# Kernel tuning notes

Hardware: AMD Instinct MI355X
Metric: run time of the kernel (lower is better)

Reference implementation:

```python
import jax, jax.numpy as jnp
import numpy as np

N_NODES = 100000
N_EDGES = 1600000
IN_F = 256
OUT_F = 128


def setup_inputs() -> dict:
    key = jax.random.key(0)
    ks = jax.random.split(key, 6)
    stdv = 1.0 / np.sqrt(OUT_F)
    x = jax.random.normal(ks[0], (N_NODES, IN_F), dtype=jnp.float32)
    edge_row = jax.random.randint(ks[1], (N_EDGES,), 0, N_NODES)
    edge_col = jax.random.randint(ks[2], (N_EDGES,), 0, N_NODES)
    edge_val = jax.random.uniform(ks[3], (N_EDGES,), dtype=jnp.float32)
    weight = jax.random.uniform(ks[4], (IN_F, OUT_F), minval=-stdv, maxval=stdv, dtype=jnp.float32)
    bias = jax.random.uniform(ks[5], (OUT_F,), minval=-stdv, maxval=stdv, dtype=jnp.float32)
    return {"x": x, "edge_row": edge_row, "edge_col": edge_col,
            "edge_val": edge_val, "weight": weight, "bias": bias}


def reference(x, edge_row, edge_col, edge_val, weight, bias):
    # support = input @ W                       [N, out]
    support = x @ weight
    # output = spmm(adj, support): for each edge (r, c, v),
    # out[r] += v * support[c]  -- gather then segment-sum over destinations.
    gathered = support[edge_col] * edge_val[:, None]   # [E, out]
    out = jax.ops.segment_sum(gathered, edge_row, num_segments=N_NODES)
    return out + bias
```

## Files before the change

### kernel.cpp

```cpp
#include <hip/hip_runtime.h>
#include <hip/hip_bf16.h>

#define N_NODES 100000
#define N_EDGES 1600000
#define IN_F 256
#define OUT_F 128

#define NBUCK 782
#define CH 4096
#define NCHB ((N_EDGES + CH - 1) / CH)
#define HCAP 2048
#define BCAP 3072

typedef __attribute__((ext_vector_type(8))) short bhalf8;
typedef __attribute__((ext_vector_type(4))) float f32x4;

static __device__ __forceinline__ unsigned short f2bfs(float f) {
    __hip_bfloat16 h = __float2bfloat16(f);
    return *reinterpret_cast<unsigned short*>(&h);
}

__global__ __launch_bounds__(256) void wt_kernel(
    const float* __restrict__ W, unsigned short* __restrict__ Wt)
{
    const int idx = blockIdx.x * 256 + threadIdx.x;
    const int col = idx >> 8;
    const int k   = idx & 255;
    Wt[idx] = f2bfs(W[(size_t)k * OUT_F + col]);
}

__global__ __launch_bounds__(512) void gemm_mfma_kernel(
    const float* __restrict__ x, const unsigned short* __restrict__ Wt,
    unsigned short* __restrict__ support)
{
    __shared__ unsigned short Bs[128 * 256];

    const int tid = threadIdx.x;

    {
        const int row = tid >> 2;
        const int q   = tid & 3;
        const uint4* src = (const uint4*)(Wt + (size_t)row * 256);
        uint4* dst       = (uint4*)(Bs + (size_t)row * 256);
        const int sw = row & 7;
        #pragma unroll
        for (int i = q * 8; i < q * 8 + 8; ++i)
            dst[i ^ sw] = src[i];
    }
    __syncthreads();

    const int wave = tid >> 6, lane = tid & 63;
    const int r_lo = lane & 15;
    const int kq   = lane >> 4;
    const int row0 = blockIdx.x * 128 + wave * 16;
    const int row  = row0 + r_lo;

    const float* xa = x + (size_t)min(row, N_NODES - 1) * IN_F + kq * 8;

    f32x4 acc[8];
    #pragma unroll
    for (int c = 0; c < 8; ++c) acc[c] = (f32x4)0.f;

    #pragma unroll
    for (int ks = 0; ks < 8; ++ks) {
        const float4 al = *(const float4*)(xa + ks * 32);
        const float4 ah = *(const float4*)(xa + ks * 32 + 4);

        bhalf8 A;
        A[0] = (short)f2bfs(al.x); A[1] = (short)f2bfs(al.y);
        A[2] = (short)f2bfs(al.z); A[3] = (short)f2bfs(al.w);
        A[4] = (short)f2bfs(ah.x); A[5] = (short)f2bfs(ah.y);
        A[6] = (short)f2bfs(ah.z); A[7] = (short)f2bfs(ah.w);

        #pragma unroll
        for (int cf = 0; cf < 8; ++cf) {
            const int col = cf * 16 + r_lo;
            const int off = ((ks * 32 + kq * 8) ^ ((col & 7) << 3));
            const bhalf8 B = *(const bhalf8*)(Bs + (size_t)col * 256 + off);
            acc[cf] = __builtin_amdgcn_mfma_f32_16x16x32_bf16(B, A, acc[cf], 0, 0, 0);
        }
    }

    if (row < N_NODES) {
        unsigned short* dst = support + (size_t)row * OUT_F + kq * 4;
        #pragma unroll
        for (int cf = 0; cf < 8; ++cf) {
            ushort4 s4;
            s4.x = f2bfs(acc[cf][0]);
            s4.y = f2bfs(acc[cf][1]);
            s4.z = f2bfs(acc[cf][2]);
            s4.w = f2bfs(acc[cf][3]);
            *(ushort4*)(dst + cf * 16) = s4;
        }
    }
}

__global__ __launch_bounds__(512) void bscatter_kernel(
    const int* __restrict__ erow, const int* __restrict__ ecol,
    const float* __restrict__ eval, int* __restrict__ bcnt,
    int2* __restrict__ ebuf)
{
    __shared__ int h[NBUCK];
    __shared__ int cur[NBUCK];
    __shared__ int gbase[NBUCK];
    __shared__ int ps[512];
    __shared__ unsigned short bb[CH];
    __shared__ int2 buf[CH];

    const int tid = threadIdx.x;
    const int e0  = blockIdx.x * CH;
    const int e1  = min(e0 + CH, N_EDGES);
    const int n   = e1 - e0;

    for (int i = tid; i < NBUCK; i += 512) h[i] = 0;
    __syncthreads();

    for (int e = e0 + tid; e < e1; e += 512)
        atomicAdd(&h[erow[e] >> 7], 1);
    __syncthreads();

    {
        const int idx0 = tid * 2;
        int sum = 0;
        #pragma unroll
        for (int k = 0; k < 2; ++k) { const int ii = idx0 + k; if (ii < NBUCK) sum += h[ii]; }
        ps[tid] = sum;
        __syncthreads();
        for (int off = 1; off < 512; off <<= 1) {
            const int a  = (tid >= off) ? ps[tid - off] : 0;
            const int x0 = ps[tid];
            __syncthreads();
            ps[tid] = x0 + a;
            __syncthreads();
        }
        int run = (tid == 0) ? 0 : ps[tid - 1];
        #pragma unroll
        for (int k = 0; k < 2; ++k) {
            const int ii = idx0 + k;
            if (ii < NBUCK) { cur[ii] = run; run += h[ii]; }
        }
    }
    __syncthreads();

    for (int e = e0 + tid; e < e1; e += 512) {
        const int r = erow[e];
        const int b = r >> 7;
        const int p = atomicAdd(&cur[b], 1);
        buf[p] = make_int2(((r & 127) << 17) | ecol[e], __float_as_int(eval[e]));
        bb[p]  = (unsigned short)b;
    }
    __syncthreads();

    for (int i = tid; i < NBUCK; i += 512)
        gbase[i] = h[i] ? (i * BCAP + atomicAdd(&bcnt[i], h[i])) : 0;
    __syncthreads();

    for (int i = tid; i < n; i += 512) {
        const int b  = bb[i];
        const int lb = cur[b] - h[b];
        ebuf[gbase[b] + (i - lb)] = buf[i];
    }
}

__global__ __launch_bounds__(256) void hspmm_kernel(
    const int* __restrict__ bcnt, const int2* __restrict__ ebuf,
    const unsigned short* __restrict__ support,
    const float* __restrict__ bias, float* __restrict__ out)
{
    __shared__ int2 srt[HCAP];
    __shared__ int rc[64];
    __shared__ int rb[65];
    __shared__ int cc[64];

    const int blk = blockIdx.x;
    const int pb  = blk >> 1;
    const unsigned hf = blk & 1;
    const int row0 = (pb << 7) + ((int)hf << 6);
    if (row0 >= N_NODES) return;
    const int nrows = min(64, N_NODES - row0);

    const int tid  = threadIdx.x;
    const int lane = tid & 63;
    const int grp  = tid >> 4;
    const int l4   = tid & 15;

    const int beg = pb * BCAP;
    const int end = beg + bcnt[pb];

    if (tid < 64) rc[tid] = 0;
    __syncthreads();

    for (int i = beg + tid; i < end; i += 256) {
        const unsigned ex = (unsigned)ebuf[i].x;
        const unsigned lr7 = (ex >> 17) & 127u;
        if ((lr7 >> 6) == hf) atomicAdd(&rc[lr7 & 63], 1);
    }
    __syncthreads();

    if (tid < 64) {
        int v = rc[tid];
        #pragma unroll
        for (int off = 1; off < 64; off <<= 1) {
            const int t = __shfl_up(v, off);
            if (lane >= off) v += t;
        }
        rb[tid + 1] = v;
        cc[tid] = v - rc[tid];
        if (tid == 0) rb[0] = 0;
    }
    __syncthreads();

    for (int i = beg + tid; i < end; i += 256) {
        const int2 e = ebuf[i];
        const unsigned lr7 = ((unsigned)e.x >> 17) & 127u;
        if ((lr7 >> 6) == hf)
            srt[atomicAdd(&cc[lr7 & 63], 1)] = e;
    }
    __syncthreads();

#define ACC(V, U)                                            \
    a0 += (V) * __uint_as_float((U).x << 16);                \
    a1 += (V) * __uint_as_float((U).x & 0xFFFF0000u);        \
    a2 += (V) * __uint_as_float((U).y << 16);                \
    a3 += (V) * __uint_as_float((U).y & 0xFFFF0000u);        \
    a4 += (V) * __uint_as_float((U).z << 16);                \
    a5 += (V) * __uint_as_float((U).z & 0xFFFF0000u);        \
    a6 += (V) * __uint_as_float((U).w << 16);                \
    a7 += (V) * __uint_as_float((U).w & 0xFFFF0000u);

    const float4 bv0 = *(const float4*)(bias + l4 * 8);
    const float4 bv1 = *(const float4*)(bias + l4 * 8 + 4);

    for (int lr = grp; lr < nrows; lr += 16) {
        const int s  = rb[lr];
        const int t2 = rb[lr + 1];
        float a0 = 0.f, a1 = 0.f, a2 = 0.f, a3 = 0.f;
        float a4 = 0.f, a5 = 0.f, a6 = 0.f, a7 = 0.f;
        int j = s;
        for (; j + 4 <= t2; j += 4) {
            const int2 e0 = srt[j],     e1 = srt[j + 1];
            const int2 e2 = srt[j + 2], e3 = srt[j + 3];
            const uint4 u0 = *(const uint4*)(support + ((size_t)(e0.x & 0x1FFFF) << 7) + l4 * 8);
            const uint4 u1 = *(const uint4*)(support + ((size_t)(e1.x & 0x1FFFF) << 7) + l4 * 8);
            const uint4 u2 = *(const uint4*)(support + ((size_t)(e2.x & 0x1FFFF) << 7) + l4 * 8);
            const uint4 u3 = *(const uint4*)(support + ((size_t)(e3.x & 0x1FFFF) << 7) + l4 * 8);
            const float v0 = __int_as_float(e0.y), v1 = __int_as_float(e1.y);
            const float v2 = __int_as_float(e2.y), v3 = __int_as_float(e3.y);
            ACC(v0, u0) ACC(v1, u1) ACC(v2, u2) ACC(v3, u3)
        }
        for (; j < t2; ++j) {
            const int2 e = srt[j];
            const uint4 u = *(const uint4*)(support + ((size_t)(e.x & 0x1FFFF) << 7) + l4 * 8);
            const float v = __int_as_float(e.y);
            ACC(v, u)
        }
        float4* o = (float4*)(out + ((size_t)(row0 + lr) << 7) + l4 * 8);
        o[0] = make_float4(a0 + bv0.x, a1 + bv0.y, a2 + bv0.z, a3 + bv0.w);
        o[1] = make_float4(a4 + bv1.x, a5 + bv1.y, a6 + bv1.z, a7 + bv1.w);
    }
#undef ACC
}

extern "C" void kernel_launch(void* const* d_in, const int* in_sizes, int n_in,
                              void* d_out, int out_size, void* d_ws, size_t ws_size,
                              hipStream_t stream) {
    const float* x    = (const float*)d_in[0];
    const int*   erow = (const int*)  d_in[1];
    const int*   ecol = (const int*)  d_in[2];
    const float* eval = (const float*)d_in[3];
    const float* W    = (const float*)d_in[4];
    const float* bias = (const float*)d_in[5];
    float*       out  = (float*)d_out;

    char* ws = (char*)d_ws;
    unsigned short* support = (unsigned short*)ws; ws += (size_t)N_NODES * OUT_F * 2;
    unsigned short* Wt      = (unsigned short*)ws; ws += (size_t)OUT_F * IN_F * 2;
    int*  bcnt  = (int*)ws;                        ws += 3136;
    int2* ebuf  = (int2*)ws;                       ws += (size_t)NBUCK * BCAP * 8;

    hipMemsetAsync(bcnt, 0, NBUCK * 4, stream);

    wt_kernel<<<(OUT_F * IN_F) / 256, 256, 0, stream>>>(W, Wt);
    gemm_mfma_kernel<<<(N_NODES + 127) / 128, 512, 0, stream>>>(x, Wt, support);

    bscatter_kernel<<<NCHB, 512, 0, stream>>>(erow, ecol, eval, bcnt, ebuf);

    hspmm_kernel<<<NBUCK * 2, 256, 0, stream>>>(bcnt, ebuf, support, bias, out);
}
```

Before: 135.3 us.

## Merge GEMM and edge bucket-scatter into one heterogeneous launch

Combines the MFMA GEMM kernel and the edge bucket-scatter kernel into a single launch. The first block range does the scatter and the rest do the GEMM, sharing one 64KB shared-memory union. The two independent stages can then run concurrently on the GPU and one kernel-launch boundary goes away. In exchange, every block reserves the full 64KB of shared memory, which can lower occupancy for the scatter blocks.

```diff
diff --git a/kernel.cpp b/kernel.cpp
--- a/kernel.cpp
+++ b/kernel.cpp
@@ -8,7 +8,8 @@
 
 #define NBUCK 782
 #define CH 4096
-#define NCHB ((N_EDGES + CH - 1) / CH)
+#define NSCAT ((N_EDGES + CH - 1) / CH)
+#define NGEMM ((N_NODES + 127) / 128)
 #define HCAP 2048
 #define BCAP 3072
 
@@ -29,136 +30,135 @@
     Wt[idx] = f2bfs(W[(size_t)k * OUT_F + col]);
 }
 
-__global__ __launch_bounds__(512) void gemm_mfma_kernel(
+__global__ __launch_bounds__(512) void fused_kernel(
     const float* __restrict__ x, const unsigned short* __restrict__ Wt,
-    unsigned short* __restrict__ support)
-{
-    __shared__ unsigned short Bs[128 * 256];
-
-    const int tid = threadIdx.x;
-
-    {
-        const int row = tid >> 2;
-        const int q   = tid & 3;
-        const uint4* src = (const uint4*)(Wt + (size_t)row * 256);
-        uint4* dst       = (uint4*)(Bs + (size_t)row * 256);
-        const int sw = row & 7;
-        #pragma unroll
-        for (int i = q * 8; i < q * 8 + 8; ++i)
-            dst[i ^ sw] = src[i];
-    }
-    __syncthreads();
-
-    const int wave = tid >> 6, lane = tid & 63;
-    const int r_lo = lane & 15;
-    const int kq   = lane >> 4;
-    const int row0 = blockIdx.x * 128 + wave * 16;
-    const int row  = row0 + r_lo;
-
-    const float* xa = x + (size_t)min(row, N_NODES - 1) * IN_F + kq * 8;
-
-    f32x4 acc[8];
-    #pragma unroll
-    for (int c = 0; c < 8; ++c) acc[c] = (f32x4)0.f;
-
-    #pragma unroll
-    for (int ks = 0; ks < 8; ++ks) {
-        const float4 al = *(const float4*)(xa + ks * 32);
-        const float4 ah = *(const float4*)(xa + ks * 32 + 4);
-
-        bhalf8 A;
-        A[0] = (short)f2bfs(al.x); A[1] = (short)f2bfs(al.y);
-        A[2] = (short)f2bfs(al.z); A[3] = (short)f2bfs(al.w);
-        A[4] = (short)f2bfs(ah.x); A[5] = (short)f2bfs(ah.y);
-        A[6] = (short)f2bfs(ah.z); A[7] = (short)f2bfs(ah.w);
-
-        #pragma unroll
-        for (int cf = 0; cf < 8; ++cf) {
-            const int col = cf * 16 + r_lo;
-            const int off = ((ks * 32 + kq * 8) ^ ((col & 7) << 3));
-            const bhalf8 B = *(const bhalf8*)(Bs + (size_t)col * 256 + off);
-            acc[cf] = __builtin_amdgcn_mfma_f32_16x16x32_bf16(B, A, acc[cf], 0, 0, 0);
-        }
-    }
-
-    if (row < N_NODES) {
-        unsigned short* dst = support + (size_t)row * OUT_F + kq * 4;
-        #pragma unroll
-        for (int cf = 0; cf < 8; ++cf) {
-            ushort4 s4;
-            s4.x = f2bfs(acc[cf][0]);
-            s4.y = f2bfs(acc[cf][1]);
-            s4.z = f2bfs(acc[cf][2]);
-            s4.w = f2bfs(acc[cf][3]);
-            *(ushort4*)(dst + cf * 16) = s4;
-        }
-    }
-}
-
-__global__ __launch_bounds__(512) void bscatter_kernel(
+    unsigned short* __restrict__ support,
     const int* __restrict__ erow, const int* __restrict__ ecol,
     const float* __restrict__ eval, int* __restrict__ bcnt,
     int2* __restrict__ ebuf)
 {
-    __shared__ int h[NBUCK];
-    __shared__ int cur[NBUCK];
-    __shared__ int gbase[NBUCK];
-    __shared__ int ps[512];
-    __shared__ unsigned short bb[CH];
-    __shared__ int2 buf[CH];
-
+    __shared__ __align__(16) char smem[65536];
     const int tid = threadIdx.x;
-    const int e0  = blockIdx.x * CH;
-    const int e1  = min(e0 + CH, N_EDGES);
-    const int n   = e1 - e0;
-
-    for (int i = tid; i < NBUCK; i += 512) h[i] = 0;
-    __syncthreads();
-
-    for (int e = e0 + tid; e < e1; e += 512)
-        atomicAdd(&h[erow[e] >> 7], 1);
-    __syncthreads();
-
-    {
-        const int idx0 = tid * 2;
-        int sum = 0;
+
+    if (blockIdx.x < NSCAT) {
+        int2*           buf   = (int2*)smem;
+        unsigned short* bb    = (unsigned short*)(smem + 32768);
+        int*            h     = (int*)(smem + 40960);
+        int*            cur   = (int*)(smem + 44096);
+        int*            gbase = (int*)(smem + 47232);
+        int*            ps    = (int*)(smem + 50368);
+
+        const int e0 = blockIdx.x * CH;
+        const int e1 = min(e0 + CH, N_EDGES);
+        const int n  = e1 - e0;
+
+        for (int i = tid; i < NBUCK; i += 512) h[i] = 0;
+        __syncthreads();
+
+        for (int e = e0 + tid; e < e1; e += 512)
+            atomicAdd(&h[erow[e] >> 7], 1);
+        __syncthreads();
+
+        {
+            const int idx0 = tid * 2;
+            int sum = 0;
+            #pragma unroll
+            for (int k = 0; k < 2; ++k) { const int ii = idx0 + k; if (ii < NBUCK) sum += h[ii]; }
+            ps[tid] = sum;
+            __syncthreads();
+            for (int off = 1; off < 512; off <<= 1) {
+                const int a  = (tid >= off) ? ps[tid - off] : 0;
+                const int x0 = ps[tid];
+                __syncthreads();
+                ps[tid] = x0 + a;
+                __syncthreads();
+            }
+            int run = (tid == 0) ? 0 : ps[tid - 1];
+            #pragma unroll
+            for (int k = 0; k < 2; ++k) {
+                const int ii = idx0 + k;
+                if (ii < NBUCK) { cur[ii] = run; run += h[ii]; }
+            }
+        }
+        __syncthreads();
+
+        for (int e = e0 + tid; e < e1; e += 512) {
+            const int r = erow[e];
+            const int b = r >> 7;
+            const int p = atomicAdd(&cur[b], 1);
+            buf[p] = make_int2(((r & 127) << 17) | ecol[e], __float_as_int(eval[e]));
+            bb[p]  = (unsigned short)b;
+        }
+        __syncthreads();
+
+        for (int i = tid; i < NBUCK; i += 512)
+            gbase[i] = h[i] ? (i * BCAP + atomicAdd(&bcnt[i], h[i])) : 0;
+        __syncthreads();
+
+        for (int i = tid; i < n; i += 512) {
+            const int b  = bb[i];
+            const int lb = cur[b] - h[b];
+            ebuf[gbase[b] + (i - lb)] = buf[i];
+        }
+    } else {
+        unsigned short* Bs = (unsigned short*)smem;
+
+        {
+            const int row = tid >> 2;
+            const int q   = tid & 3;
+            const uint4* src = (const uint4*)(Wt + (size_t)row * 256);
+            uint4* dst       = (uint4*)(Bs + (size_t)row * 256);
+            const int sw = row & 7;
+            #pragma unroll
+            for (int i = q * 8; i < q * 8 + 8; ++i)
+                dst[i ^ sw] = src[i];
+        }
+        __syncthreads();
+
+        const int wave = tid >> 6, lane = tid & 63;
+        const int r_lo = lane & 15;
+        const int kq   = lane >> 4;
+        const int row0 = (blockIdx.x - NSCAT) * 128 + wave * 16;
+        const int row  = row0 + r_lo;
+
+        const float* xa = x + (size_t)min(row, N_NODES - 1) * IN_F + kq * 8;
+
+        f32x4 acc[8];
         #pragma unroll
-        for (int k = 0; k < 2; ++k) { const int ii = idx0 + k; if (ii < NBUCK) sum += h[ii]; }
-        ps[tid] = sum;
-        __syncthreads();
-        for (int off = 1; off < 512; off <<= 1) {
-            const int a  = (tid >= off) ? ps[tid - off] : 0;
-            const int x0 = ps[tid];
-            __syncthreads();
-            ps[tid] = x0 + a;
-            __syncthreads();
-        }
-        int run = (tid == 0) ? 0 : ps[tid - 1];
+        for (int c = 0; c < 8; ++c) acc[c] = (f32x4)0.f;
+
         #pragma unroll
-        for (int k = 0; k < 2; ++k) {
-            const int ii = idx0 + k;
-            if (ii < NBUCK) { cur[ii] = run; run += h[ii]; }
-        }
-    }
-    __syncthreads();
-
-    for (int e = e0 + tid; e < e1; e += 512) {
-        const int r = erow[e];
-        const int b = r >> 7;
-        const int p = atomicAdd(&cur[b], 1);
-        buf[p] = make_int2(((r & 127) << 17) | ecol[e], __float_as_int(eval[e]));
-        bb[p]  = (unsigned short)b;
-    }
-    __syncthreads();
-
-    for (int i = tid; i < NBUCK; i += 512)
-        gbase[i] = h[i] ? (i * BCAP + atomicAdd(&bcnt[i], h[i])) : 0;
-    __syncthreads();
-
-    for (int i = tid; i < n; i += 512) {
-        const int b  = bb[i];
-        const int lb = cur[b] - h[b];
-        ebuf[gbase[b] + (i - lb)] = buf[i];
+        for (int ks = 0; ks < 8; ++ks) {
+            const float4 al = *(const float4*)(xa + ks * 32);
+            const float4 ah = *(const float4*)(xa + ks * 32 + 4);
+
+            bhalf8 A;
+            A[0] = (short)f2bfs(al.x); A[1] = (short)f2bfs(al.y);
+            A[2] = (short)f2bfs(al.z); A[3] = (short)f2bfs(al.w);
+            A[4] = (short)f2bfs(ah.x); A[5] = (short)f2bfs(ah.y);
+            A[6] = (short)f2bfs(ah.z); A[7] = (short)f2bfs(ah.w);
+
+            #pragma unroll
+            for (int cf = 0; cf < 8; ++cf) {
+                const int col = cf * 16 + r_lo;
+                const int off = ((ks * 32 + kq * 8) ^ ((col & 7) << 3));
+                const bhalf8 B = *(const bhalf8*)(Bs + (size_t)col * 256 + off);
+                acc[cf] = __builtin_amdgcn_mfma_f32_16x16x32_bf16(B, A, acc[cf], 0, 0, 0);
+            }
+        }
+
+        if (row < N_NODES) {
+            unsigned short* dst = support + (size_t)row * OUT_F + kq * 4;
+            #pragma unroll
+            for (int cf = 0; cf < 8; ++cf) {
+                ushort4 s4;
+                s4.x = f2bfs(acc[cf][0]);
+                s4.y = f2bfs(acc[cf][1]);
+                s4.z = f2bfs(acc[cf][2]);
+                s4.w = f2bfs(acc[cf][3]);
+                *(ushort4*)(dst + cf * 16) = s4;
+            }
+        }
     }
 }
 
@@ -281,9 +281,9 @@
     hipMemsetAsync(bcnt, 0, NBUCK * 4, stream);
 
     wt_kernel<<<(OUT_F * IN_F) / 256, 256, 0, stream>>>(W, Wt);
-    gemm_mfma_kernel<<<(N_NODES + 127) / 128, 512, 0, stream>>>(x, Wt, support);
-
-    bscatter_kernel<<<NCHB, 512, 0, stream>>>(erow, ecol, eval, bcnt, ebuf);
+
+    fused_kernel<<<NSCAT + NGEMM, 512, 0, stream>>>(
+        x, Wt, support, erow, ecol, eval, bcnt, ebuf);
 
     hspmm_kernel<<<NBUCK * 2, 256, 0, stream>>>(bcnt, ebuf, support, bias, out);
 }
```

New measurement: 122.9 us. -9.2%, faster.
